# Kernel tuning notes

Hardware: AMD Instinct MI355X
Metric: run time of the kernel (lower is better)

Reference implementation:

```python
import jax, jax.numpy as jnp
import numpy as np

N_NODES = 100000
N_EDGES = 1000000
DIM = 128
N_RELS = 500
N_TIMES = 1000


def setup_inputs() -> dict:
    key = jax.random.key(0)
    ks = jax.random.split(key, 8)
    h = jax.random.normal(ks[0], (N_NODES, DIM), dtype=jnp.float32)
    edge_index = jax.random.randint(ks[1], (2, N_EDGES), 0, N_NODES, dtype=jnp.int64)
    edge_type = jax.random.randint(ks[2], (N_EDGES,), 0, N_RELS, dtype=jnp.int64)
    edge_time = jax.random.randint(ks[3], (N_EDGES,), 0, N_TIMES, dtype=jnp.int64)
    query_rel = 7
    rel_table = jax.random.normal(ks[4], (N_RELS, DIM), dtype=jnp.float32)
    time_table = jax.random.normal(ks[5], (N_TIMES, DIM), dtype=jnp.float32)
    # Linear weights stored as [in, out] so y = x @ W + b
    W1 = jax.random.normal(ks[6], (4 * DIM, DIM), dtype=jnp.float32) * (1.0 / np.sqrt(4 * DIM))
    b1 = jnp.zeros((DIM,), dtype=jnp.float32)
    W2 = jax.random.normal(ks[7], (DIM, 1), dtype=jnp.float32) * (1.0 / np.sqrt(DIM))
    b2 = jnp.zeros((1,), dtype=jnp.float32)
    return {"h": h, "edge_index": edge_index, "edge_type": edge_type,
            "edge_time": edge_time, "query_rel": query_rel,
            "rel_table": rel_table, "time_table": time_table,
            "W1": W1, "b1": b1, "W2": W2, "b2": b2}


def reference(h, edge_index, edge_type, edge_time, query_rel,
              rel_table, time_table, W1, b1, W2, b2):
    src = edge_index[0]                    # [E]
    h_s = h[src]                           # [E, D] gather
    h_r = rel_table[edge_type]             # [E, D] embedding lookup
    h_t = time_table[edge_time]            # [E, D] embedding lookup
    h_rq = jnp.broadcast_to(rel_table[query_rel][None, :], h_s.shape)  # [E, D]
    x = jnp.concatenate([h_s, h_r, h_rq, h_t], axis=1)  # [E, 4D]
    hidden = jax.nn.relu(x @ W1 + b1)      # [E, D]
    alpha = hidden @ W2 + b2               # [E, 1]
    return jax.nn.sigmoid(alpha)[:, 0]     # [E]
```

## Files before the change

### kernel.cpp

```cpp
#include <hip/hip_runtime.h>
#include <hip/hip_fp16.h>
#include <hip/hip_fp8.h>
#include <math.h>

#define DIM 128

typedef _Float16 half8 __attribute__((ext_vector_type(8)));
typedef _Float16 half2v __attribute__((ext_vector_type(2)));
typedef float floatx4 __attribute__((ext_vector_type(4)));


__global__ __launch_bounds__(256) void precompute(
    const float* __restrict__ h, const float* __restrict__ rel,
    const float* __restrict__ tim, const int* __restrict__ qrel,
    const float* __restrict__ W1, const float* __restrict__ b1,
    unsigned char* __restrict__ H8, __half* __restrict__ Rh, __half* __restrict__ Th,
    int n_nodes, int n_rels, int n_times, int nHB, int nRB)
{
    const int tid = threadIdx.x;
    const int b = blockIdx.x;

    const float* A; int M, k0, row0; bool isR = false, isH = false;
    __half* Out = nullptr;
    if (b < nHB)            { A = h;   isH = true; M = n_nodes; k0 = 0;   row0 = b * 128; }
    else if (b < nHB + nRB) { A = rel; Out = Rh;   M = n_rels;  k0 = 128; row0 = (b - nHB) * 128; isR = true; }
    else                    { A = tim; Out = Th;   M = n_times; k0 = 384; row0 = (b - nHB - nRB) * 128; }

    __shared__ _Float16 fragB[32 * 64 * 8];
    __shared__ float c0f[DIM];

#pragma unroll
    for (int it = 0; it < 8; ++it) {
        const int o = tid + it * 256;
        const int ctkc = o >> 6, L = o & 63;
        const int ct = ctkc >> 2, kc = ctkc & 3;
        const int q = L >> 4, n15 = L & 15;
        const float* base = W1 + (size_t)(k0 + kc * 32 + q * 8) * DIM + ct * 16 + n15;
        half8 f;
#pragma unroll
        for (int j = 0; j < 8; ++j) f[j] = (_Float16)base[(size_t)j * DIM];
        *(half8*)&fragB[o * 8] = f;
    }
    if (isR && tid < DIM) {
        const int q = qrel[0];
        const float* hq = rel + (size_t)q * DIM;
        float s = b1[tid];
        for (int k = 0; k < DIM; ++k)
            s = fmaf(hq[k], W1[(size_t)(256 + k) * DIM + tid], s);
        c0f[tid] = s;
    }
    __syncthreads();

    const int w = tid >> 6;
    const int lane = tid & 63;
    const int m15 = lane & 15, q = lane >> 4;

    const float* aBase[2];
#pragma unroll
    for (int mt = 0; mt < 2; ++mt) {
        int arow = row0 + w * 32 + mt * 16 + m15;
        if (arow >= M) arow = M - 1;
        aBase[mt] = A + (size_t)arow * DIM + q * 8;
    }

    floatx4 acc[2][8];
#pragma unroll
    for (int mt = 0; mt < 2; ++mt)
#pragma unroll
        for (int ct = 0; ct < 8; ++ct) acc[mt][ct] = (floatx4)0.f;

#pragma unroll
    for (int kc = 0; kc < 4; ++kc) {
        half8 af[2];
#pragma unroll
        for (int mt = 0; mt < 2; ++mt) {
            const float4 a0 = *(const float4*)(aBase[mt] + kc * 32);
            const float4 a1 = *(const float4*)(aBase[mt] + kc * 32 + 4);
            af[mt][0] = (_Float16)a0.x; af[mt][1] = (_Float16)a0.y;
            af[mt][2] = (_Float16)a0.z; af[mt][3] = (_Float16)a0.w;
            af[mt][4] = (_Float16)a1.x; af[mt][5] = (_Float16)a1.y;
            af[mt][6] = (_Float16)a1.z; af[mt][7] = (_Float16)a1.w;
        }
#pragma unroll
        for (int ct = 0; ct < 8; ++ct) {
            const half8 bf = *(half8*)&fragB[(((ct * 4 + kc) * 64) + lane) * 8];
            acc[0][ct] = __builtin_amdgcn_mfma_f32_16x16x32_f16(af[0], bf, acc[0][ct], 0, 0, 0);
            acc[1][ct] = __builtin_amdgcn_mfma_f32_16x16x32_f16(af[1], bf, acc[1][ct], 0, 0, 0);
        }
    }

    float cadd[8];
#pragma unroll
    for (int ct = 0; ct < 8; ++ct) cadd[ct] = isR ? c0f[ct * 16 + m15] : 0.f;

#pragma unroll
    for (int mt = 0; mt < 2; ++mt)
#pragma unroll
        for (int r = 0; r < 4; ++r) {
            const int m = row0 + w * 32 + mt * 16 + q * 4 + r;
            if (m < M) {
                if (isH) {
                    uint2 pk;
#if __has_builtin(__builtin_amdgcn_cvt_pk_fp8_f32)
                    int w0 = 0, w1 = 0;
                    w0 = __builtin_amdgcn_cvt_pk_fp8_f32(acc[mt][0][r], acc[mt][1][r], w0, false);
                    w0 = __builtin_amdgcn_cvt_pk_fp8_f32(acc[mt][2][r], acc[mt][3][r], w0, true);
                    w1 = __builtin_amdgcn_cvt_pk_fp8_f32(acc[mt][4][r], acc[mt][5][r], w1, false);
                    w1 = __builtin_amdgcn_cvt_pk_fp8_f32(acc[mt][6][r], acc[mt][7][r], w1, true);
                    pk.x = (unsigned)w0; pk.y = (unsigned)w1;
#else
                    union { uint2 u; unsigned char bb[8]; } pu;
#pragma unroll
                    for (int ct = 0; ct < 8; ++ct)
                        pu.bb[ct] = __hip_fp8_e4m3(acc[mt][ct][r]).__x;
                    pk = pu.u;
#endif
                    *(uint2*)(H8 + (size_t)m * DIM + m15 * 8) = pk;
                } else {
                    half8 hv;
#pragma unroll
                    for (int ct = 0; ct < 8; ++ct)
                        hv[ct] = (_Float16)(acc[mt][ct][r] + cadd[ct]);
                    *(half8*)(Out + (size_t)m * DIM + m15 * 8) = hv;
                }
            }
        }
}

__device__ __forceinline__ half2v fp8x2_to_h2(unsigned u16) {
#if __has_builtin(__builtin_amdgcn_cvt_pk_f16_fp8)
    auto c = __builtin_amdgcn_cvt_pk_f16_fp8((short)u16);
    half2v r; r[0] = c[0]; r[1] = c[1];
    return r;
#else
    auto f = __builtin_amdgcn_cvt_pk_f32_fp8((int)u16, false);
    half2v r; r[0] = (_Float16)f[0]; r[1] = (_Float16)f[1];
    return r;
#endif
}

__device__ __forceinline__ float edot(uint2 hu, uint4 ru, uint4 tu,
                                      const half2v* __restrict__ w2h) {
    union U { uint4 u; half2v h[4]; };
    U R, T; R.u = ru; T.u = tu;
    const half2v z = (half2v)(_Float16)0.f;
    const unsigned hw[4] = {hu.x & 0xffffu, hu.x >> 16, hu.y & 0xffffu, hu.y >> 16};
    float p = 0.f;
#pragma unroll
    for (int j = 0; j < 4; ++j) {
        const half2v hh = fp8x2_to_h2(hw[j]);
        half2v s = hh + R.h[j] + T.h[j];
        s = __builtin_elementwise_max(s, z);
#if __has_builtin(__builtin_amdgcn_fdot2)
        p = __builtin_amdgcn_fdot2(s, w2h[j], p, false);
#else
        p = fmaf((float)s[0], (float)w2h[j][0], p);
        p = fmaf((float)s[1], (float)w2h[j][1], p);
#endif
    }
    return p;
}

__global__ __launch_bounds__(256) void edge_kernel(
    const int* __restrict__ ei, const int* __restrict__ ety,
    const int* __restrict__ eti,
    const unsigned char* __restrict__ H8, const __half* __restrict__ Rh,
    const __half* __restrict__ Th,
    const float* __restrict__ W2, const float* __restrict__ b2,
    float* __restrict__ out, int E, int nGrpTotal)
{
    const int tid = threadIdx.x;
    const int l = tid & 15;
    int g = blockIdx.x * 16 + (tid >> 4);
    const int nQuad = (E + 3) >> 2;
    if (g >= nQuad) return;

    half2v w2h[4];
#pragma unroll
    for (int j = 0; j < 4; ++j) {
        w2h[j][0] = (_Float16)W2[(2 * j) * 16 + l];
        w2h[j][1] = (_Float16)W2[(2 * j + 1) * 16 + l];
    }
    const float b2v = b2[0];
    const bool exact = (E & 3) == 0;

    int s[4], r[4], t[4];
    {
        const int e0 = 4 * g;
        if (exact || e0 + 3 < E) {
#pragma unroll
            for (int i = 0; i < 4; ++i) { s[i] = ei[e0 + i]; r[i] = ety[e0 + i]; t[i] = eti[e0 + i]; }
        } else {
#pragma unroll
            for (int i = 0; i < 4; ++i) {
                const int e = min(e0 + i, E - 1);
                s[i] = ei[e]; r[i] = ety[e]; t[i] = eti[e];
            }
        }
    }

    while (true) {
        const int gn = g + nGrpTotal;
        uint2 hv[4]; uint4 rv[4], tv[4];
#pragma unroll
        for (int i = 0; i < 4; ++i) {
            hv[i] = ((const uint2*)(H8 + (size_t)s[i] * DIM))[l];
            rv[i] = ((const uint4*)(Rh + (size_t)r[i] * DIM))[l];
            tv[i] = ((const uint4*)(Th + (size_t)t[i] * DIM))[l];
        }
        if (gn < nQuad) {
            const int e0 = 4 * gn;
            if (exact || e0 + 3 < E) {
#pragma unroll
                for (int i = 0; i < 4; ++i) { s[i] = ei[e0 + i]; r[i] = ety[e0 + i]; t[i] = eti[e0 + i]; }
            } else {
#pragma unroll
                for (int i = 0; i < 4; ++i) {
                    const int e = min(e0 + i, E - 1);
                    s[i] = ei[e]; r[i] = ety[e]; t[i] = eti[e];
                }
            }
        }
        float p[4];
#pragma unroll
        for (int i = 0; i < 4; ++i)
            p[i] = edot(hv[i], rv[i], tv[i], w2h);
#pragma unroll
        for (int off = 8; off > 0; off >>= 1) {
#pragma unroll
            for (int i = 0; i < 4; ++i)
                p[i] += __shfl_down(p[i], off, 16);
        }
        if (l == 0) {
            const int e0 = 4 * g;
            float4 o;
            o.x = 1.f / (1.f + __expf(-(p[0] + b2v)));
            o.y = 1.f / (1.f + __expf(-(p[1] + b2v)));
            o.z = 1.f / (1.f + __expf(-(p[2] + b2v)));
            o.w = 1.f / (1.f + __expf(-(p[3] + b2v)));
            if (e0 + 3 < E) {
                *(float4*)(out + e0) = o;
            } else {
                const float ov[4] = {o.x, o.y, o.z, o.w};
                for (int i = 0; i < 4 && e0 + i < E; ++i) out[e0 + i] = ov[i];
            }
        }
        if (gn >= nQuad) break;
        g = gn;
    }
}

extern "C" void kernel_launch(void* const* d_in, const int* in_sizes, int n_in,
                              void* d_out, int out_size, void* d_ws, size_t ws_size,
                              hipStream_t stream) {
    const float* h          = (const float*)d_in[0];
    const int*   edge_index = (const int*)d_in[1];
    const int*   edge_type  = (const int*)d_in[2];
    const int*   edge_time  = (const int*)d_in[3];
    const int*   query_rel  = (const int*)d_in[4];
    const float* rel_table  = (const float*)d_in[5];
    const float* time_table = (const float*)d_in[6];
    const float* W1         = (const float*)d_in[7];
    const float* b1         = (const float*)d_in[8];
    const float* W2         = (const float*)d_in[9];
    const float* b2         = (const float*)d_in[10];
    float* out = (float*)d_out;

    const int n_nodes = in_sizes[0] / DIM;
    const int E       = in_sizes[2];
    const int n_rels  = in_sizes[5] / DIM;
    const int n_times = in_sizes[6] / DIM;

    unsigned char* H8 = (unsigned char*)d_ws;
    __half* Rh = (__half*)(H8 + (((size_t)n_nodes * DIM + 255) & ~(size_t)255));
    __half* Th = Rh + (size_t)n_rels * DIM;

    const int nHB = (n_nodes + 127) / 128;
    const int nRB = (n_rels + 127) / 128;
    const int nTB = (n_times + 127) / 128;

    precompute<<<nHB + nRB + nTB, 256, 0, stream>>>(
        h, rel_table, time_table, query_rel, W1, b1,
        H8, Rh, Th, n_nodes, n_rels, n_times, nHB, nRB);

    const int nBlk = 4096;
    edge_kernel<<<nBlk, 256, 0, stream>>>(
        edge_index, edge_type, edge_time, H8, Rh, Th, W2, b2,
        out, E, nBlk * 16);
}
```

Before: 159.9 us.

## Double-buffer edge gathers and use DPP row reductions in edge kernel

Restructures the edge kernel's grid-stride loop into a two-stage ping-pong pipeline. The gathers for the next quad of edges are issued before the current quad is computed, and index loads run two iterations ahead, so memory latency overlaps with compute. The 16-lane shuffle reduction is replaced with DPP row_shr adds, which leaves the result in lane 15, and the grid is halved to 2048 blocks. This costs extra registers for the two buffers, which may reduce occupancy.

```diff
diff --git a/kernel.cpp b/kernel.cpp
--- a/kernel.cpp
+++ b/kernel.cpp
@@ -161,6 +161,76 @@
     return p;
 }
 
+template<int CTRL>
+__device__ __forceinline__ float dpp_row_add(float x) {
+    int s = __builtin_amdgcn_update_dpp(0, __float_as_int(x), CTRL, 0xf, 0xf, true);
+    return x + __int_as_float(s);
+}
+
+__device__ __forceinline__ void load_idx(
+    const int* __restrict__ ei, const int* __restrict__ ety,
+    const int* __restrict__ eti, int g, int E, bool exact,
+    int (&s)[4], int (&r)[4], int (&t)[4])
+{
+    const int e0 = 4 * g;
+    if (exact || e0 + 3 < E) {
+#pragma unroll
+        for (int i = 0; i < 4; ++i) { s[i] = ei[e0 + i]; r[i] = ety[e0 + i]; t[i] = eti[e0 + i]; }
+    } else {
+#pragma unroll
+        for (int i = 0; i < 4; ++i) {
+            const int e = min(e0 + i, E - 1);
+            s[i] = ei[e]; r[i] = ety[e]; t[i] = eti[e];
+        }
+    }
+}
+
+__device__ __forceinline__ void issue_gather(
+    const unsigned char* __restrict__ H8, const unsigned char* __restrict__ Rh8,
+    const unsigned char* __restrict__ Th8, int l,
+    const int (&s)[4], const int (&r)[4], const int (&t)[4],
+    uint2 (&hv)[4], uint4 (&rv)[4], uint4 (&tv)[4])
+{
+#pragma unroll
+    for (int i = 0; i < 4; ++i) {
+        hv[i] = *(const uint2*)(H8 + ((unsigned)s[i] << 7) + (l << 3));
+        rv[i] = *(const uint4*)(Rh8 + ((unsigned)r[i] << 8) + (l << 4));
+        tv[i] = *(const uint4*)(Th8 + ((unsigned)t[i] << 8) + (l << 4));
+    }
+}
+
+__device__ __forceinline__ void compute_store(
+    int g, int l, int E,
+    const uint2 (&hv)[4], const uint4 (&rv)[4], const uint4 (&tv)[4],
+    const half2v (&w2h)[4], float b2v, float* __restrict__ out)
+{
+    float p[4];
+#pragma unroll
+    for (int i = 0; i < 4; ++i)
+        p[i] = edot(hv[i], rv[i], tv[i], w2h);
+#pragma unroll
+    for (int i = 0; i < 4; ++i) {
+        p[i] = dpp_row_add<0x111>(p[i]);
+        p[i] = dpp_row_add<0x112>(p[i]);
+        p[i] = dpp_row_add<0x114>(p[i]);
+        p[i] = dpp_row_add<0x118>(p[i]);
+    }
+    if (l == 15) {
+        const int e0 = 4 * g;
+        float4 o;
+        o.x = 1.f / (1.f + __expf(-(p[0] + b2v)));
+        o.y = 1.f / (1.f + __expf(-(p[1] + b2v)));
+        o.z = 1.f / (1.f + __expf(-(p[2] + b2v)));
+        o.w = 1.f / (1.f + __expf(-(p[3] + b2v)));
+        if (e0 + 3 < E) {
+            *(float4*)(out + e0) = o;
+        } else {
+            const float ov[4] = {o.x, o.y, o.z, o.w};
+            for (int i = 0; i < 4 && e0 + i < E; ++i) out[e0 + i] = ov[i];
+        }
+    }
+}
+
 __global__ __launch_bounds__(256) void edge_kernel(
     const int* __restrict__ ei, const int* __restrict__ ety,
     const int* __restrict__ eti,
@@ -171,9 +241,9 @@
 {
     const int tid = threadIdx.x;
     const int l = tid & 15;
-    int g = blockIdx.x * 16 + (tid >> 4);
     const int nQuad = (E + 3) >> 2;
-    if (g >= nQuad) return;
+    int g0 = blockIdx.x * 16 + (tid >> 4);
+    if (g0 >= nQuad) return;
 
     half2v w2h[4];
 #pragma unroll
@@ -183,70 +253,35 @@
     }
     const float b2v = b2[0];
     const bool exact = (E & 3) == 0;
-
-    int s[4], r[4], t[4];
-    {
-        const int e0 = 4 * g;
-        if (exact || e0 + 3 < E) {
-#pragma unroll
-            for (int i = 0; i < 4; ++i) { s[i] = ei[e0 + i]; r[i] = ety[e0 + i]; t[i] = eti[e0 + i]; }
-        } else {
-#pragma unroll
-            for (int i = 0; i < 4; ++i) {
-                const int e = min(e0 + i, E - 1);
-                s[i] = ei[e]; r[i] = ety[e]; t[i] = eti[e];
-            }
-        }
-    }
+    const unsigned char* Rh8 = (const unsigned char*)Rh;
+    const unsigned char* Th8 = (const unsigned char*)Th;
+
+    int sA[4], rA[4], tA[4], sB[4], rB[4], tB[4];
+    uint2 hA[4], hB[4];
+    uint4 rvA[4], tvA[4], rvB[4], tvB[4];
+
+    load_idx(ei, ety, eti, g0, E, exact, sA, rA, tA);
+    issue_gather(H8, Rh8, Th8, l, sA, rA, tA, hA, rvA, tvA);
+    int g1 = g0 + nGrpTotal;
+    bool h1 = g1 < nQuad;
+    if (h1) load_idx(ei, ety, eti, g1, E, exact, sB, rB, tB);
 
     while (true) {
-        const int gn = g + nGrpTotal;
-        uint2 hv[4]; uint4 rv[4], tv[4];
-#pragma unroll
-        for (int i = 0; i < 4; ++i) {
-            hv[i] = ((const uint2*)(H8 + (size_t)s[i] * DIM))[l];
-            rv[i] = ((const uint4*)(Rh + (size_t)r[i] * DIM))[l];
-            tv[i] = ((const uint4*)(Th + (size_t)t[i] * DIM))[l];
-        }
-        if (gn < nQuad) {
-            const int e0 = 4 * gn;
-            if (exact || e0 + 3 < E) {
-#pragma unroll
-                for (int i = 0; i < 4; ++i) { s[i] = ei[e0 + i]; r[i] = ety[e0 + i]; t[i] = eti[e0 + i]; }
-            } else {
-#pragma unroll
-                for (int i = 0; i < 4; ++i) {
-                    const int e = min(e0 + i, E - 1);
-                    s[i] = ei[e]; r[i] = ety[e]; t[i] = eti[e];
-                }
-            }
-        }
-        float p[4];
-#pragma unroll
-        for (int i = 0; i < 4; ++i)
-            p[i] = edot(hv[i], rv[i], tv[i], w2h);
-#pragma unroll
-        for (int off = 8; off > 0; off >>= 1) {
-#pragma unroll
-            for (int i = 0; i < 4; ++i)
-                p[i] += __shfl_down(p[i], off, 16);
-        }
-        if (l == 0) {
-            const int e0 = 4 * g;
-            float4 o;
-            o.x = 1.f / (1.f + __expf(-(p[0] + b2v)));
-            o.y = 1.f / (1.f + __expf(-(p[1] + b2v)));
-            o.z = 1.f / (1.f + __expf(-(p[2] + b2v)));
-            o.w = 1.f / (1.f + __expf(-(p[3] + b2v)));
-            if (e0 + 3 < E) {
-                *(float4*)(out + e0) = o;
-            } else {
-                const float ov[4] = {o.x, o.y, o.z, o.w};
-                for (int i = 0; i < 4 && e0 + i < E; ++i) out[e0 + i] = ov[i];
-            }
-        }
-        if (gn >= nQuad) break;
-        g = gn;
+        if (h1) issue_gather(H8, Rh8, Th8, l, sB, rB, tB, hB, rvB, tvB);
+        int g2 = g1 + nGrpTotal;
+        bool h2 = h1 && (g2 < nQuad);
+        if (h2) load_idx(ei, ety, eti, g2, E, exact, sA, rA, tA);
+        compute_store(g0, l, E, hA, rvA, tvA, w2h, b2v, out);
+        if (!h1) break;
+
+        if (h2) issue_gather(H8, Rh8, Th8, l, sA, rA, tA, hA, rvA, tvA);
+        int g3 = g2 + nGrpTotal;
+        bool h3 = h2 && (g3 < nQuad);
+        if (h3) load_idx(ei, ety, eti, g3, E, exact, sB, rB, tB);
+        compute_store(g1, l, E, hB, rvB, tvB, w2h, b2v, out);
+        if (!h2) break;
+
+        g0 = g2; g1 = g3; h1 = h3;
     }
 }
 
@@ -283,7 +318,7 @@
         h, rel_table, time_table, query_rel, W1, b1,
         H8, Rh, Th, n_nodes, n_rels, n_times, nHB, nRB);
 
-    const int nBlk = 4096;
+    const int nBlk = 2048;
     edge_kernel<<<nBlk, 256, 0, stream>>>(
         edge_index, edge_type, edge_time, H8, Rh, Th, W2, b2,
         out, E, nBlk * 16);
```

New measurement: 161.6 us. Within noise of the previous version (+1.1%).
